# Optimization experiments

Measured on AMD Instinct MI355X. Metric: run time of the kernel, lower is better.

## Reference

```python
import jax, jax.numpy as jnp
import numpy as np

N_NODES = 100000

def gin_conv(x, edge_index, W, b):
    # PyG GINConv with eps=0: out = Linear(x + sum_{j->i} x_j)
    src, dst = edge_index[0], edge_index[1]
    agg = jax.ops.segment_sum(x[src], dst, num_segments=N_NODES)  # [N, d]
    return (x + agg) @ W + b

def setup_inputs() -> dict:
    key = jax.random.key(0)
    ks = jax.random.split(key, 8)
    x = jax.random.normal(ks[0], (N_NODES, 32), dtype=jnp.float32)
    edge_index = jax.random.randint(ks[1], (2, 1600000), 0, N_NODES, dtype=jnp.int64)
    def lin(k, fan_in, fan_out):
        kw, kb = jax.random.split(k)
        lim = 1.0 / np.sqrt(fan_in)
        W = jax.random.uniform(kw, (fan_in, fan_out), minval=-lim, maxval=lim, dtype=jnp.float32)
        b = jax.random.uniform(kb, (fan_out,), minval=-lim, maxval=lim, dtype=jnp.float32)
        return W, b
    W1, b1 = lin(ks[2], 32, 64)
    W2, b2 = lin(ks[3], 64, 64)
    W3, b3 = lin(ks[4], 64, 10)
    return {"x": x, "edge_index": edge_index,
            "W1": W1, "b1": b1, "W2": W2, "b2": b2, "W3": W3, "b3": b3}

def reference(x, edge_index, W1, b1, W2, b2, W3, b3):
    h = jax.nn.relu(gin_conv(x, edge_index, W1, b1))
    h = jax.nn.relu(gin_conv(h, edge_index, W2, b2))
    return gin_conv(h, edge_index, W3, b3)  # [N, classes] logits
```

## Files before the change

kernel.cpp:

```cpp
#include <hip/hip_runtime.h>


#define GIN_N 100000
#define NBUCKET 256
#define NB2 391
#define BSTRIDE 8192
#define EPT 16

typedef unsigned short bfu;
typedef float v2f __attribute__((ext_vector_type(2)));

__device__ __forceinline__ float bf_lo(unsigned int u) {
    return __uint_as_float(u << 16);
}
__device__ __forceinline__ float bf_hi(unsigned int u) {
    return __uint_as_float(u & 0xffff0000u);
}
__device__ __forceinline__ unsigned int f2bf(float f) {
    unsigned int u = __float_as_uint(f);
    return (u + 0x7fffu + ((u >> 16) & 1u)) >> 16;
}
__device__ __forceinline__ v2f fp8lo(unsigned u) {
    return __builtin_amdgcn_cvt_pk_f32_fp8(u, false);
}
__device__ __forceinline__ v2f fp8hi(unsigned u) {
    return __builtin_amdgcn_cvt_pk_f32_fp8(u, true);
}

template <int S>
__device__ __forceinline__ void blelloch_excl(int* a) {
#pragma unroll
    for (int d = 1; d < S; d <<= 1) {
        __syncthreads();
        int idx = (threadIdx.x + 1) * (d << 1) - 1;
        if (idx < S) a[idx] += a[idx - d];
    }
    __syncthreads();
    if (threadIdx.x == 0) a[S - 1] = 0;
#pragma unroll
    for (int d = S >> 1; d >= 1; d >>= 1) {
        __syncthreads();
        int idx = (threadIdx.x + 1) * (d << 1) - 1;
        if (idx < S) {
            int t = a[idx - d];
            a[idx - d] = a[idx];
            a[idx] += t;
        }
    }
    __syncthreads();
}

__global__ __launch_bounds__(256) void build_kernel(
        const int* __restrict__ src, const int* __restrict__ dst, int E,
        unsigned* __restrict__ bucketbuf, int* __restrict__ cursor,
        const float* __restrict__ x, unsigned* __restrict__ xq, int n8,
        int bblk) {
    __shared__ int h[NBUCKET];
    __shared__ int base[NBUCKET];
    int tid = threadIdx.x;
    if (blockIdx.x >= bblk) {
        int t = (blockIdx.x - bblk) * 256 + tid;
        if (t >= n8) return;
        const float4* v = reinterpret_cast<const float4*>(x);
        float4 a = v[2 * t], b = v[2 * t + 1];
        unsigned w0 = 0, w1 = 0;
        w0 = __builtin_amdgcn_cvt_pk_fp8_f32(a.x, a.y, w0, false);
        w0 = __builtin_amdgcn_cvt_pk_fp8_f32(a.z, a.w, w0, true);
        w1 = __builtin_amdgcn_cvt_pk_fp8_f32(b.x, b.y, w1, false);
        w1 = __builtin_amdgcn_cvt_pk_fp8_f32(b.z, b.w, w1, true);
        reinterpret_cast<uint2*>(xq)[t] = make_uint2(w0, w1);
        return;
    }
    int chunk0 = blockIdx.x * (256 * EPT);
    h[tid] = 0;
    __syncthreads();
    int myb[EPT];
    unsigned myrec[EPT];
#pragma unroll
    for (int i = 0; i < EPT; ++i) {
        int e = chunk0 + tid + i * 256;
        if (e < E) {
            int d = dst[e];
            int s = src[e];
            int b = d / NB2;
            myb[i] = b;
            myrec[i] = ((unsigned)(d - b * NB2) << 17) | (unsigned)s;
            atomicAdd(&h[b], 1);
        } else {
            myb[i] = -1;
        }
    }
    __syncthreads();
    base[tid] = atomicAdd(&cursor[tid], h[tid]);
    h[tid] = 0;
    __syncthreads();
#pragma unroll
    for (int i = 0; i < EPT; ++i) {
        int b = myb[i];
        if (b < 0) continue;
        int pos = base[b] + atomicAdd(&h[b], 1);
        if (pos < BSTRIDE) bucketbuf[(size_t)b * BSTRIDE + pos] = myrec[i];
    }
}

__global__ __launch_bounds__(256) void csr_build_kernel(
        const unsigned* __restrict__ bucketbuf,
        const int* __restrict__ cursor,
        int* __restrict__ rowptr,
        int* __restrict__ adj) {
    __shared__ int csr[BSTRIDE];
    __shared__ int cnt[512];
    __shared__ int off[512];
    __shared__ int bscan[NBUCKET];
    int b = blockIdx.x;
    int tid = threadIdx.x;
    bscan[tid] = cursor[tid];
    int mycnt = cursor[b];
    if (mycnt > BSTRIDE) mycnt = BSTRIDE;
    blelloch_excl<NBUCKET>(bscan);
    int base = bscan[b];

    const unsigned* buf = bucketbuf + (size_t)b * BSTRIDE;
    cnt[tid] = 0;
    cnt[tid + 256] = 0;
    __syncthreads();
    for (int i = tid; i < mycnt; i += 256)
        atomicAdd(&cnt[buf[i] >> 17], 1);
    __syncthreads();
    off[tid] = cnt[tid];
    off[tid + 256] = cnt[tid + 256];
    blelloch_excl<512>(off);

    int nodes0 = b * NB2;
    int nn2 = GIN_N + 1 - nodes0;
    if (nn2 > NB2) nn2 = NB2;
    for (int l = tid; l < nn2; l += 256) rowptr[nodes0 + l] = base + off[l];
    __syncthreads();

    for (int i = tid; i < mycnt; i += 256) {
        unsigned r = buf[i];
        int pos = atomicAdd(&off[r >> 17], 1);
        csr[pos] = (int)(r & 0x1FFFFu);
    }
    __syncthreads();
    for (int i = tid; i < mycnt; i += 256) adj[base + i] = csr[i];
}

__global__ __launch_bounds__(256, 8) void fused1_kernel(
        const float* __restrict__ xf,
        const unsigned* __restrict__ xq,
        const int* __restrict__ rowptr,
        const int* __restrict__ adj,
        const float* __restrict__ W,
        const float* __restrict__ b,
        unsigned* __restrict__ outq) {
    constexpr int K = 32, M = 64;
    constexpr int TPN = 4, NODES = 64, TP2 = 4, MT = 16;
    constexpr int STR = K + 4;

    __shared__ unsigned Wp[K * M / 2];
    __shared__ float bs[M];
    __shared__ float tile[NODES * STR];

    for (int i = threadIdx.x; i < K * M / 2; i += 256) {
        float w0 = W[2 * i], w1 = W[2 * i + 1];
        Wp[i] = f2bf(w0) | (f2bf(w1) << 16);
    }
    if (threadIdx.x < M) bs[threadIdx.x] = b[threadIdx.x];

    int node0 = blockIdx.x * NODES;
    int tid = threadIdx.x;

    {
        int l = tid / TPN;
        int j = tid % TPN;
        int n = node0 + l;
        if (n < GIN_N) {
            int start = rowptr[n];
            int d = rowptr[n + 1] - start;
            const int* row = adj + start;
            const uint2* fq = reinterpret_cast<const uint2*>(xq);
            v2f a0, a1, a2, a3;
            {
                const float4* xv = reinterpret_cast<const float4*>(xf);
                float4 a = xv[(size_t)n * 8 + 2 * j];
                float4 c = xv[(size_t)n * 8 + 2 * j + 1];
                a0 = v2f{a.x, a.y}; a1 = v2f{a.z, a.w};
                a2 = v2f{c.x, c.y}; a3 = v2f{c.z, c.w};
            }
#define ACC8(v) { a0 += fp8lo(v.x); a1 += fp8hi(v.x); \
                  a2 += fp8lo(v.y); a3 += fp8hi(v.y); }
            int k = 0;
            for (; k + 8 <= d; k += 8) {
                uint2 v0 = fq[(size_t)row[k] * 4 + j];
                uint2 v1 = fq[(size_t)row[k + 1] * 4 + j];
                uint2 v2 = fq[(size_t)row[k + 2] * 4 + j];
                uint2 v3 = fq[(size_t)row[k + 3] * 4 + j];
                uint2 v4 = fq[(size_t)row[k + 4] * 4 + j];
                uint2 v5 = fq[(size_t)row[k + 5] * 4 + j];
                uint2 v6 = fq[(size_t)row[k + 6] * 4 + j];
                uint2 v7 = fq[(size_t)row[k + 7] * 4 + j];
                ACC8(v0) ACC8(v1) ACC8(v2) ACC8(v3)
                ACC8(v4) ACC8(v5) ACC8(v6) ACC8(v7)
            }
            for (; k + 4 <= d; k += 4) {
                uint2 v0 = fq[(size_t)row[k] * 4 + j];
                uint2 v1 = fq[(size_t)row[k + 1] * 4 + j];
                uint2 v2 = fq[(size_t)row[k + 2] * 4 + j];
                uint2 v3 = fq[(size_t)row[k + 3] * 4 + j];
                ACC8(v0) ACC8(v1) ACC8(v2) ACC8(v3)
            }
            for (; k < d; ++k) {
                uint2 v = fq[(size_t)row[k] * 4 + j];
                ACC8(v)
            }
#undef ACC8
            float* tp = &tile[l * STR + j * 8];
            tp[0] = a0.x; tp[1] = a0.y; tp[2] = a1.x; tp[3] = a1.y;
            tp[4] = a2.x; tp[5] = a2.y; tp[6] = a3.x; tp[7] = a3.y;
        }
    }
    __syncthreads();

    {
        int l = tid / TP2;
        int sub = tid % TP2;
        int n = node0 + l;
        if (n >= GIN_N) return;
        float acc[MT];
#pragma unroll
        for (int jj = 0; jj < MT; ++jj) acc[jj] = bs[sub * MT + jj];
        const float* tp = &tile[l * STR];
#pragma unroll
        for (int k = 0; k < K; ++k) {
            float v = tp[k];
            const unsigned* wr = &Wp[k * (M / 2) + sub * (MT / 2)];
#pragma unroll
            for (int j2 = 0; j2 < MT / 2; ++j2) {
                unsigned wp = wr[j2];
                acc[2 * j2]     = fmaf(v, bf_lo(wp), acc[2 * j2]);
                acc[2 * j2 + 1] = fmaf(v, bf_hi(wp), acc[2 * j2 + 1]);
            }
        }
#pragma unroll
        for (int jj = 0; jj < MT; ++jj) acc[jj] = fmaxf(acc[jj], 0.0f);
        unsigned q[4];
#pragma unroll
        for (int q4 = 0; q4 < 4; ++q4) {
            unsigned w = 0;
            w = __builtin_amdgcn_cvt_pk_fp8_f32(acc[4 * q4], acc[4 * q4 + 1], w, false);
            w = __builtin_amdgcn_cvt_pk_fp8_f32(acc[4 * q4 + 2], acc[4 * q4 + 3], w, true);
            q[q4] = w;
        }
        reinterpret_cast<uint4*>(outq)[(size_t)n * 4 + sub] =
            make_uint4(q[0], q[1], q[2], q[3]);
    }
}

__global__ __launch_bounds__(256, 8) void fused2t_kernel(
        const unsigned* __restrict__ xq,
        const int* __restrict__ rowptr,
        const int* __restrict__ adj,
        const float* __restrict__ W,
        const float* __restrict__ b,
        const float* __restrict__ W3,
        unsigned* __restrict__ tout) {
    constexpr int K = 64, M = 64;
    constexpr int TPN = 8, NODES = 32, TP2 = 8, MT = 8;
    constexpr int STR = K + 4;

    __shared__ unsigned Wp[K * M / 2];
    __shared__ float bs[M];
    __shared__ float W3t[10 * K];
    __shared__ float tile[NODES * STR];

    for (int i = threadIdx.x; i < K * M / 2; i += 256) {
        float w0 = W[2 * i], w1 = W[2 * i + 1];
        Wp[i] = f2bf(w0) | (f2bf(w1) << 16);
    }
    for (int i = threadIdx.x; i < 10 * K; i += 256) {
        int jj = i >> 6, k = i & 63;
        W3t[i] = W3[k * 10 + jj];
    }
    if (threadIdx.x < M) bs[threadIdx.x] = b[threadIdx.x];

    int node0 = blockIdx.x * NODES;
    int tid = threadIdx.x;

    {
        int l = tid / TPN;
        int j = tid % TPN;
        int n = node0 + l;
        if (n < GIN_N) {
            int start = rowptr[n];
            int d = rowptr[n + 1] - start;
            const int* row = adj + start;
            const uint2* fq = reinterpret_cast<const uint2*>(xq);
            v2f a0, a1, a2, a3;
            {
                uint2 s = fq[(size_t)n * 8 + j];
                a0 = fp8lo(s.x); a1 = fp8hi(s.x);
                a2 = fp8lo(s.y); a3 = fp8hi(s.y);
            }
#define ACC8(v) { a0 += fp8lo(v.x); a1 += fp8hi(v.x); \
                  a2 += fp8lo(v.y); a3 += fp8hi(v.y); }
            int k = 0;
            for (; k + 8 <= d; k += 8) {
                uint2 v0 = fq[(size_t)row[k] * 8 + j];
                uint2 v1 = fq[(size_t)row[k + 1] * 8 + j];
                uint2 v2 = fq[(size_t)row[k + 2] * 8 + j];
                uint2 v3 = fq[(size_t)row[k + 3] * 8 + j];
                uint2 v4 = fq[(size_t)row[k + 4] * 8 + j];
                uint2 v5 = fq[(size_t)row[k + 5] * 8 + j];
                uint2 v6 = fq[(size_t)row[k + 6] * 8 + j];
                uint2 v7 = fq[(size_t)row[k + 7] * 8 + j];
                ACC8(v0) ACC8(v1) ACC8(v2) ACC8(v3)
                ACC8(v4) ACC8(v5) ACC8(v6) ACC8(v7)
            }
            for (; k + 4 <= d; k += 4) {
                uint2 v0 = fq[(size_t)row[k] * 8 + j];
                uint2 v1 = fq[(size_t)row[k + 1] * 8 + j];
                uint2 v2 = fq[(size_t)row[k + 2] * 8 + j];
                uint2 v3 = fq[(size_t)row[k + 3] * 8 + j];
                ACC8(v0) ACC8(v1) ACC8(v2) ACC8(v3)
            }
            for (; k < d; ++k) {
                uint2 v = fq[(size_t)row[k] * 8 + j];
                ACC8(v)
            }
#undef ACC8
            float* tp = &tile[l * STR + j * 8];
            tp[0] = a0.x; tp[1] = a0.y; tp[2] = a1.x; tp[3] = a1.y;
            tp[4] = a2.x; tp[5] = a2.y; tp[6] = a3.x; tp[7] = a3.y;
        }
    }
    __syncthreads();

    {
        int l = tid / TP2;
        int sub = tid % TP2;
        int n = node0 + l;
        if (n >= GIN_N) return;
        float acc[MT];
#pragma unroll
        for (int jj = 0; jj < MT; ++jj) acc[jj] = bs[sub * MT + jj];
        const float* tp = &tile[l * STR];
#pragma unroll
        for (int k = 0; k < K; ++k) {
            float v = tp[k];
            const unsigned* wr = &Wp[k * (M / 2) + sub * (MT / 2)];
#pragma unroll
            for (int j2 = 0; j2 < MT / 2; ++j2) {
                unsigned wp = wr[j2];
                acc[2 * j2]     = fmaf(v, bf_lo(wp), acc[2 * j2]);
                acc[2 * j2 + 1] = fmaf(v, bf_hi(wp), acc[2 * j2 + 1]);
            }
        }
#pragma unroll
        for (int jj = 0; jj < MT; ++jj) acc[jj] = fmaxf(acc[jj], 0.0f);
        float pt[10];
#pragma unroll
        for (int jj = 0; jj < 10; ++jj) {
            const float* wr = &W3t[jj * K + sub * MT];
            float v = acc[0] * wr[0];
#pragma unroll
            for (int kk = 1; kk < MT; ++kk) v = fmaf(acc[kk], wr[kk], v);
            pt[jj] = v;
        }
#pragma unroll
        for (int jj = 0; jj < 10; ++jj) {
            float v = pt[jj];
            v += __shfl_xor(v, 1, 64);
            v += __shfl_xor(v, 2, 64);
            v += __shfl_xor(v, 4, 64);
            pt[jj] = v;
        }
        if (sub == 0) {
            unsigned p[8];
#pragma unroll
            for (int j2 = 0; j2 < 5; ++j2)
                p[j2] = f2bf(pt[2 * j2]) | (f2bf(pt[2 * j2 + 1]) << 16);
            p[5] = 0; p[6] = 0; p[7] = 0;
            uint4* o = reinterpret_cast<uint4*>(tout) + (size_t)n * 2;
            o[0] = make_uint4(p[0], p[1], p[2], p[3]);
            o[1] = make_uint4(p[4], p[5], p[6], p[7]);
        }
    }
}

__global__ void gather_final_kernel(const unsigned* __restrict__ t8,
                                    const int* __restrict__ rowptr,
                                    const int* __restrict__ adj,
                                    const float* __restrict__ b3,
                                    float* __restrict__ out) {
    int t = blockIdx.x * blockDim.x + threadIdx.x;
    int n = t >> 3;
    int j = t & 7;
    if (n >= GIN_N || j >= 5) return;
    int start = rowptr[n];
    int d = rowptr[n + 1] - start;
    const int* row = adj + start;
    unsigned sv = t8[(size_t)n * 8 + j];
    float a0 = bf_lo(sv), a1 = bf_hi(sv);
    int k = 0;
    for (; k + 4 <= d; k += 4) {
        int r0 = row[k], r1 = row[k + 1], r2 = row[k + 2], r3 = row[k + 3];
        unsigned v0 = t8[(size_t)r0 * 8 + j];
        unsigned v1 = t8[(size_t)r1 * 8 + j];
        unsigned v2 = t8[(size_t)r2 * 8 + j];
        unsigned v3 = t8[(size_t)r3 * 8 + j];
        a0 += bf_lo(v0) + bf_lo(v1) + bf_lo(v2) + bf_lo(v3);
        a1 += bf_hi(v0) + bf_hi(v1) + bf_hi(v2) + bf_hi(v3);
    }
    for (; k < d; ++k) {
        unsigned v = t8[(size_t)row[k] * 8 + j];
        a0 += bf_lo(v); a1 += bf_hi(v);
    }
    out[(size_t)n * 10 + 2 * j] = a0 + b3[2 * j];
    out[(size_t)n * 10 + 2 * j + 1] = a1 + b3[2 * j + 1];
}

extern "C" void kernel_launch(void* const* d_in, const int* in_sizes, int n_in,
                              void* d_out, int out_size, void* d_ws, size_t ws_size,
                              hipStream_t stream) {
    const float* x  = (const float*)d_in[0];
    const int*   ei = (const int*)d_in[1];
    const float* W1 = (const float*)d_in[2];
    const float* b1 = (const float*)d_in[3];
    const float* W2 = (const float*)d_in[4];
    const float* b2 = (const float*)d_in[5];
    const float* W3 = (const float*)d_in[6];
    const float* b3 = (const float*)d_in[7];
    float* out = (float*)d_out;

    const int N = GIN_N;
    const int E = in_sizes[1] / 2;
    const int* src = ei;
    const int* dst = ei + E;

    unsigned* Xq = (unsigned*)d_ws;
    unsigned* H1q = Xq + (size_t)N * 8;
    unsigned* Tb = H1q + (size_t)N * 16;
    int* rowptr = (int*)(Tb + (size_t)N * 8);
    int* cursor = rowptr + (N + 8);
    int* adj = cursor + 256;
    unsigned* bucketbuf = (unsigned*)(adj + (size_t)E);

    const int BLK = 256;

    hipMemsetAsync(cursor, 0, 256 * sizeof(int), stream);
    {
        int n8 = N * 32 / 8;
        int bblk = (E + BLK * EPT - 1) / (BLK * EPT);
        int xblk = (n8 + BLK - 1) / BLK;
        build_kernel<<<bblk + xblk, BLK, 0, stream>>>(
            src, dst, E, bucketbuf, cursor, x, Xq, n8, bblk);
        csr_build_kernel<<<NBUCKET, BLK, 0, stream>>>(
            bucketbuf, cursor, rowptr, adj);
    }

    fused1_kernel<<<(N + 63) / 64, BLK, 0, stream>>>(
        x, Xq, rowptr, adj, W1, b1, H1q);

    fused2t_kernel<<<(N + 31) / 32, BLK, 0, stream>>>(
        H1q, rowptr, adj, W2, b2, W3, Tb);

    gather_final_kernel<<<(N * 8 + BLK - 1) / BLK, BLK, 0, stream>>>(
        Tb, rowptr, adj, b3, out);
}
```

Before: 206.6 us.

## Use bf16 MFMA for dense linear layers in fused GIN kernels

Replaces the scalar FMA dense transform in both fused aggregation kernels with 16x16x32 bf16 MFMA instructions. Aggregated rows are packed to bf16 in LDS, and the weights are transposed into an MFMA-friendly padded layout. In the second kernel the W3 projection is restructured around the MFMA output layout, with cross-wave partial sums reduced through shared memory under an extra barrier. Rounding activations to bf16 before the matmul adds some precision loss, and the extra sync and shared buffers add overhead.

```diff
diff --git a/kernel.cpp b/kernel.cpp
--- a/kernel.cpp
+++ b/kernel.cpp
@@ -7,8 +7,10 @@
 #define BSTRIDE 8192
 #define EPT 16
 
-typedef unsigned short bfu;
 typedef float v2f __attribute__((ext_vector_type(2)));
+typedef float f32x4 __attribute__((ext_vector_type(4)));
+typedef short s16x8 __attribute__((ext_vector_type(8)));
+typedef unsigned int u32x4 __attribute__((ext_vector_type(4)));
 
 __device__ __forceinline__ float bf_lo(unsigned int u) {
     return __uint_as_float(u << 16);
@@ -20,11 +22,17 @@
     unsigned int u = __float_as_uint(f);
     return (u + 0x7fffu + ((u >> 16) & 1u)) >> 16;
 }
+__device__ __forceinline__ unsigned pk2bf(float lo, float hi) {
+    return f2bf(lo) | (f2bf(hi) << 16);
+}
 __device__ __forceinline__ v2f fp8lo(unsigned u) {
     return __builtin_amdgcn_cvt_pk_f32_fp8(u, false);
 }
 __device__ __forceinline__ v2f fp8hi(unsigned u) {
     return __builtin_amdgcn_cvt_pk_f32_fp8(u, true);
+}
+__device__ __forceinline__ s16x8 lds_frag(const unsigned* p) {
+    return __builtin_bit_cast(s16x8, *reinterpret_cast<const u32x4*>(p));
 }
 
 template <int S>
@@ -155,21 +163,22 @@
         const float* __restrict__ b,
         unsigned* __restrict__ outq) {
     constexpr int K = 32, M = 64;
-    constexpr int TPN = 4, NODES = 64, TP2 = 4, MT = 16;
-    constexpr int STR = K + 4;
-
-    __shared__ unsigned Wp[K * M / 2];
+    constexpr int TPN = 4, NODES = 64;
+    constexpr int KW = K / 2;
+    constexpr int WSTR = KW + 4;
+
+    __shared__ unsigned Wb[M * WSTR];
     __shared__ float bs[M];
-    __shared__ float tile[NODES * STR];
-
-    for (int i = threadIdx.x; i < K * M / 2; i += 256) {
-        float w0 = W[2 * i], w1 = W[2 * i + 1];
-        Wp[i] = f2bf(w0) | (f2bf(w1) << 16);
-    }
-    if (threadIdx.x < M) bs[threadIdx.x] = b[threadIdx.x];
+    __shared__ unsigned tile[NODES * WSTR];
+
+    int tid = threadIdx.x;
+    for (int i = tid; i < M * KW; i += 256) {
+        int k2 = i >> 6, j = i & 63;
+        Wb[j * WSTR + k2] = pk2bf(W[(2 * k2) * M + j], W[(2 * k2 + 1) * M + j]);
+    }
+    if (tid < M) bs[tid] = b[tid];
 
     int node0 = blockIdx.x * NODES;
-    int tid = threadIdx.x;
 
     {
         int l = tid / TPN;
@@ -215,45 +224,37 @@
                 ACC8(v)
             }
 #undef ACC8
-            float* tp = &tile[l * STR + j * 8];
-            tp[0] = a0.x; tp[1] = a0.y; tp[2] = a1.x; tp[3] = a1.y;
-            tp[4] = a2.x; tp[5] = a2.y; tp[6] = a3.x; tp[7] = a3.y;
-        }
-    }
-    __syncthreads();
-
-    {
-        int l = tid / TP2;
-        int sub = tid % TP2;
-        int n = node0 + l;
-        if (n >= GIN_N) return;
-        float acc[MT];
-#pragma unroll
-        for (int jj = 0; jj < MT; ++jj) acc[jj] = bs[sub * MT + jj];
-        const float* tp = &tile[l * STR];
-#pragma unroll
-        for (int k = 0; k < K; ++k) {
-            float v = tp[k];
-            const unsigned* wr = &Wp[k * (M / 2) + sub * (MT / 2)];
-#pragma unroll
-            for (int j2 = 0; j2 < MT / 2; ++j2) {
-                unsigned wp = wr[j2];
-                acc[2 * j2]     = fmaf(v, bf_lo(wp), acc[2 * j2]);
-                acc[2 * j2 + 1] = fmaf(v, bf_hi(wp), acc[2 * j2 + 1]);
-            }
-        }
-#pragma unroll
-        for (int jj = 0; jj < MT; ++jj) acc[jj] = fmaxf(acc[jj], 0.0f);
-        unsigned q[4];
-#pragma unroll
-        for (int q4 = 0; q4 < 4; ++q4) {
-            unsigned w = 0;
-            w = __builtin_amdgcn_cvt_pk_fp8_f32(acc[4 * q4], acc[4 * q4 + 1], w, false);
-            w = __builtin_amdgcn_cvt_pk_fp8_f32(acc[4 * q4 + 2], acc[4 * q4 + 3], w, true);
-            q[q4] = w;
-        }
-        reinterpret_cast<uint4*>(outq)[(size_t)n * 4 + sub] =
-            make_uint4(q[0], q[1], q[2], q[3]);
+            *reinterpret_cast<uint4*>(&tile[l * WSTR + j * 4]) = make_uint4(
+                pk2bf(a0.x, a0.y), pk2bf(a1.x, a1.y),
+                pk2bf(a2.x, a2.y), pk2bf(a3.x, a3.y));
+        }
+    }
+    __syncthreads();
+
+    {
+        int w = tid >> 6;
+        int l = tid & 63;
+        int c = l & 15;
+        int g = l >> 4;
+        int n = node0 + w * 16 + c;
+        s16x8 bf = lds_frag(&tile[(w * 16 + c) * WSTR + 4 * g]);
+#pragma unroll
+        for (int jt = 0; jt < 4; ++jt) {
+            int j0 = jt * 16;
+            s16x8 af = lds_frag(&Wb[(j0 + c) * WSTR + 4 * g]);
+            f32x4 a;
+            a.x = bs[j0 + 4 * g + 0];
+            a.y = bs[j0 + 4 * g + 1];
+            a.z = bs[j0 + 4 * g + 2];
+            a.w = bs[j0 + 4 * g + 3];
+            a = __builtin_amdgcn_mfma_f32_16x16x32_bf16(af, bf, a, 0, 0, 0);
+            float r0 = fmaxf(a.x, 0.0f), r1 = fmaxf(a.y, 0.0f);
+            float r2 = fmaxf(a.z, 0.0f), r3 = fmaxf(a.w, 0.0f);
+            unsigned u = 0;
+            u = __builtin_amdgcn_cvt_pk_fp8_f32(r0, r1, u, false);
+            u = __builtin_amdgcn_cvt_pk_fp8_f32(r2, r3, u, true);
+            if (n < GIN_N) outq[(size_t)n * 16 + jt * 4 + g] = u;
+        }
     }
 }
 
@@ -266,26 +267,28 @@
         const float* __restrict__ W3,
         unsigned* __restrict__ tout) {
     constexpr int K = 64, M = 64;
-    constexpr int TPN = 8, NODES = 32, TP2 = 8, MT = 8;
-    constexpr int STR = K + 4;
-
-    __shared__ unsigned Wp[K * M / 2];
+    constexpr int TPN = 8, NODES = 32;
+    constexpr int KW = K / 2;
+    constexpr int WSTR = KW + 4;
+
+    __shared__ unsigned Wb[M * WSTR];
     __shared__ float bs[M];
-    __shared__ float W3t[10 * K];
-    __shared__ float tile[NODES * STR];
-
-    for (int i = threadIdx.x; i < K * M / 2; i += 256) {
-        float w0 = W[2 * i], w1 = W[2 * i + 1];
-        Wp[i] = f2bf(w0) | (f2bf(w1) << 16);
-    }
-    for (int i = threadIdx.x; i < 10 * K; i += 256) {
-        int jj = i >> 6, k = i & 63;
-        W3t[i] = W3[k * 10 + jj];
-    }
-    if (threadIdx.x < M) bs[threadIdx.x] = b[threadIdx.x];
+    __shared__ float W3n[M * 12];
+    __shared__ unsigned tile[NODES * WSTR];
+    __shared__ float ptb[2][NODES][10];
+
+    int tid = threadIdx.x;
+    for (int i = tid; i < M * KW; i += 256) {
+        int k2 = i >> 6, j = i & 63;
+        Wb[j * WSTR + k2] = pk2bf(W[(2 * k2) * M + j], W[(2 * k2 + 1) * M + j]);
+    }
+    for (int i = tid; i < M * 10; i += 256) {
+        int j = i / 10, jj = i - 10 * j;
+        W3n[j * 12 + jj] = W3[i];
+    }
+    if (tid < M) bs[tid] = b[tid];
 
     int node0 = blockIdx.x * NODES;
-    int tid = threadIdx.x;
 
     {
         int l = tid / TPN;
@@ -329,62 +332,82 @@
                 ACC8(v)
             }
 #undef ACC8
-            float* tp = &tile[l * STR + j * 8];
-            tp[0] = a0.x; tp[1] = a0.y; tp[2] = a1.x; tp[3] = a1.y;
-            tp[4] = a2.x; tp[5] = a2.y; tp[6] = a3.x; tp[7] = a3.y;
-        }
-    }
-    __syncthreads();
-
-    {
-        int l = tid / TP2;
-        int sub = tid % TP2;
-        int n = node0 + l;
-        if (n >= GIN_N) return;
-        float acc[MT];
-#pragma unroll
-        for (int jj = 0; jj < MT; ++jj) acc[jj] = bs[sub * MT + jj];
-        const float* tp = &tile[l * STR];
-#pragma unroll
-        for (int k = 0; k < K; ++k) {
-            float v = tp[k];
-            const unsigned* wr = &Wp[k * (M / 2) + sub * (MT / 2)];
-#pragma unroll
-            for (int j2 = 0; j2 < MT / 2; ++j2) {
-                unsigned wp = wr[j2];
-                acc[2 * j2]     = fmaf(v, bf_lo(wp), acc[2 * j2]);
-                acc[2 * j2 + 1] = fmaf(v, bf_hi(wp), acc[2 * j2 + 1]);
-            }
-        }
-#pragma unroll
-        for (int jj = 0; jj < MT; ++jj) acc[jj] = fmaxf(acc[jj], 0.0f);
-        float pt[10];
+            *reinterpret_cast<uint4*>(&tile[l * WSTR + j * 4]) = make_uint4(
+                pk2bf(a0.x, a0.y), pk2bf(a1.x, a1.y),
+                pk2bf(a2.x, a2.y), pk2bf(a3.x, a3.y));
+        }
+    }
+    __syncthreads();
+
+    {
+        int w  = tid >> 6;
+        int l  = tid & 63;
+        int c  = l & 15;
+        int g  = l >> 4;
+        int nt = w & 1;
+        int jp = w >> 1;
+        const unsigned* trow = &tile[(nt * 16 + c) * WSTR];
+        s16x8 bf0 = lds_frag(trow + 4 * g);
+        s16x8 bf1 = lds_frag(trow + 16 + 4 * g);
+        f32x4 acc[2];
+#pragma unroll
+        for (int jt = 0; jt < 2; ++jt) {
+            int j0 = (2 * jp + jt) * 16;
+            const unsigned* arow = &Wb[(j0 + c) * WSTR];
+            s16x8 af0 = lds_frag(arow + 4 * g);
+            s16x8 af1 = lds_frag(arow + 16 + 4 * g);
+            f32x4 a;
+            a.x = bs[j0 + 4 * g + 0];
+            a.y = bs[j0 + 4 * g + 1];
+            a.z = bs[j0 + 4 * g + 2];
+            a.w = bs[j0 + 4 * g + 3];
+            a = __builtin_amdgcn_mfma_f32_16x16x32_bf16(af0, bf0, a, 0, 0, 0);
+            a = __builtin_amdgcn_mfma_f32_16x16x32_bf16(af1, bf1, a, 0, 0, 0);
+            acc[jt] = a;
+        }
+        v2f pt[5];
+#pragma unroll
+        for (int q = 0; q < 5; ++q) pt[q] = v2f{0.0f, 0.0f};
+#pragma unroll
+        for (int jt = 0; jt < 2; ++jt) {
+            int jb = (2 * jp + jt) * 16 + 4 * g;
+#pragma unroll
+            for (int r = 0; r < 4; ++r) {
+                float h = fmaxf(acc[jt][r], 0.0f);
+                const v2f* wr =
+                    reinterpret_cast<const v2f*>(&W3n[(jb + r) * 12]);
+#pragma unroll
+                for (int q = 0; q < 5; ++q) pt[q] += wr[q] * h;
+            }
+        }
+        float ptf[10];
+#pragma unroll
+        for (int q = 0; q < 5; ++q) { ptf[2 * q] = pt[q].x; ptf[2 * q + 1] = pt[q].y; }
 #pragma unroll
         for (int jj = 0; jj < 10; ++jj) {
-            const float* wr = &W3t[jj * K + sub * MT];
-            float v = acc[0] * wr[0];
-#pragma unroll
-            for (int kk = 1; kk < MT; ++kk) v = fmaf(acc[kk], wr[kk], v);
-            pt[jj] = v;
-        }
-#pragma unroll
-        for (int jj = 0; jj < 10; ++jj) {
-            float v = pt[jj];
-            v += __shfl_xor(v, 1, 64);
-            v += __shfl_xor(v, 2, 64);
-            v += __shfl_xor(v, 4, 64);
-            pt[jj] = v;
-        }
-        if (sub == 0) {
-            unsigned p[8];
-#pragma unroll
-            for (int j2 = 0; j2 < 5; ++j2)
-                p[j2] = f2bf(pt[2 * j2]) | (f2bf(pt[2 * j2 + 1]) << 16);
-            p[5] = 0; p[6] = 0; p[7] = 0;
-            uint4* o = reinterpret_cast<uint4*>(tout) + (size_t)n * 2;
-            o[0] = make_uint4(p[0], p[1], p[2], p[3]);
-            o[1] = make_uint4(p[4], p[5], p[6], p[7]);
-        }
+            float v = ptf[jj];
+            v += __shfl_xor(v, 16, 64);
+            v += __shfl_xor(v, 32, 64);
+            ptf[jj] = v;
+        }
+        if (g == 0) {
+#pragma unroll
+            for (int jj = 0; jj < 10; ++jj)
+                ptb[jp][nt * 16 + c][jj] = ptf[jj];
+        }
+    }
+    __syncthreads();
+
+    {
+        int n = tid >> 3, q = tid & 7;
+        int node = node0 + n;
+        unsigned u = 0;
+        if (q < 5) {
+            float lo = ptb[0][n][2 * q]     + ptb[1][n][2 * q];
+            float hi = ptb[0][n][2 * q + 1] + ptb[1][n][2 * q + 1];
+            u = pk2bf(lo, hi);
+        }
+        if (node < GIN_N) tout[(size_t)node * 8 + q] = u;
     }
 }
 
```

After: 186.8 us. 9.6% less time.
